# Kernel optimization log

Hardware: AMD Instinct MI355X
Metric: run time of the kernel (lower is better)

The kernel has to match this reference:

```python
import jax, jax.numpy as jnp
import numpy as np

DIM = 2048
HQ = 32
HKV = 8
HEAD_DIM = DIM // HQ          # 64
GROUP = HQ // HKV             # 4 q-heads per kv-head
B, S = 2, 2048


def setup_inputs() -> dict:
    key = jax.random.key(0)
    ks = jax.random.split(key, 12)
    sc_in = 1.0 / np.sqrt(DIM)   # lecun_normal fan-in scaling
    inp = {
        "q": jax.random.normal(ks[0], (B, S, DIM), jnp.float32),
        "k": jax.random.normal(ks[1], (B, S, DIM), jnp.float32),
        "v": jax.random.normal(ks[2], (B, S, DIM), jnp.float32),
        # causal 0/1 mask: module computes scores -= 1/mask + 1, so 0 -> -inf (masked), 1 -> -2 (softmax-invariant shift)
        "mask": jnp.tril(jnp.ones((S, S), jnp.int32)),
        "Wq": jax.random.normal(ks[3], (DIM, HQ * HEAD_DIM), jnp.float32) * sc_in,
        "bq": jnp.zeros((HQ * HEAD_DIM,), jnp.float32),
        "Wk": jax.random.normal(ks[4], (DIM, HKV * HEAD_DIM), jnp.float32) * sc_in,
        "bk": jnp.zeros((HKV * HEAD_DIM,), jnp.float32),
        "Wv": jax.random.normal(ks[5], (DIM, HKV * HEAD_DIM), jnp.float32) * sc_in,
        "bv": jnp.zeros((HKV * HEAD_DIM,), jnp.float32),
        "Wo": jax.random.normal(ks[6], (DIM, DIM), jnp.float32) * (1.0 / np.sqrt(DIM)),
        "bo": jnp.zeros((DIM,), jnp.float32),
    }
    return inp


def reference(q, k, v, mask, Wq, bq, Wk, bk, Wv, bv, Wo, bo):
    b, s, _ = q.shape
    # projections -> per-head layout
    qx = (q @ Wq + bq).reshape(b, s, HKV, GROUP, HEAD_DIM)   # grouped q-heads
    kx = (k @ Wk + bk).reshape(b, s, HKV, HEAD_DIM)
    vx = (v @ Wv + bv).reshape(b, s, HKV, HEAD_DIM)
    # scores[b, h, g, i, j] = q_i . k_j ; same math as repeating kv heads GROUP times
    scores = jnp.einsum('bihgd,bjhd->bhgij', qx, kx) / jnp.sqrt(
        jnp.asarray(HEAD_DIM, qx.dtype))
    # module's masking: scores -= 1/mask + 1  (mask==0 -> -inf, mask==1 -> -2)
    scores = scores - (1.0 / mask.astype(scores.dtype) + 1.0)
    probs = jax.nn.softmax(scores, axis=-1)
    out = jnp.einsum('bhgij,bjhd->bihgd', probs, vx).reshape(b, s, DIM)
    out = out @ Wo + bo
    return out
```

## Files before the change

kernel.cpp:

```cpp
#include <hip/hip_runtime.h>

typedef unsigned short u16;
typedef unsigned int u32;
typedef __attribute__((ext_vector_type(8))) short short8v;
typedef __attribute__((ext_vector_type(4))) float f32x4;

#define DIM 2048
#define HQN 32
#define HKVN 8
#define HD 64
#define BB 2
#define SS 2048
#define MTOT (BB*SS)
#define NKV (HKVN*HD)

__device__ __forceinline__ u16 f2bf(float f){
  u32 u = __float_as_uint(f);
  u += 0x7FFFu + ((u >> 16) & 1u);
  return (u16)(u >> 16);
}

__device__ __forceinline__ u32 cvtpk(float a, float b){
  u32 r; asm("v_cvt_pk_bf16_f32 %0, %1, %2" : "=v"(r) : "v"(a), "v"(b)); return r;
}

__device__ __forceinline__ void gload_lds16(const void* g, void* l){
  __builtin_amdgcn_global_load_lds((const __attribute__((address_space(1))) u32*)g,
                                   (__attribute__((address_space(3))) u32*)l, 16, 0, 0);
}

#define WAITVM_(N) asm volatile("s_waitcnt vmcnt(" #N ")" ::: "memory")
#define WAITVM(N) WAITVM_(N)
#define BARF()    do { asm volatile("" ::: "memory"); __builtin_amdgcn_s_barrier(); asm volatile("" ::: "memory"); } while(0)
#define MF(a,b,cc) __builtin_amdgcn_mfma_f32_16x16x32_bf16((a),(b),(cc),0,0,0)

__global__ __launch_bounds__(256) void cast3_kernel(const float4* __restrict__ q,
                                                    const float4* __restrict__ k,
                                                    const float4* __restrict__ v,
                                                    u16* __restrict__ qo,
                                                    u16* __restrict__ ko,
                                                    u16* __restrict__ vo, int n4){
  const int z = blockIdx.y;
  const float4* in = z==0 ? q : (z==1 ? k : v);
  u16* out = z==0 ? qo : (z==1 ? ko : vo);
  int i = blockIdx.x*256 + threadIdx.x;
  if (i < n4){
    float4 f = in[i];
    union { u16 s[4]; unsigned long long u; } r;
    r.s[0]=f2bf(f.x); r.s[1]=f2bf(f.y); r.s[2]=f2bf(f.z); r.s[3]=f2bf(f.w);
    *(unsigned long long*)(out + (size_t)i*4) = r.u;
  }
}

__global__ __launch_bounds__(256) void transpose4_kernel(const float* __restrict__ Wq,
                                                         const float* __restrict__ Wk,
                                                         const float* __restrict__ Wv,
                                                         const float* __restrict__ Wo,
                                                         u16* __restrict__ WqT,
                                                         u16* __restrict__ WkT,
                                                         u16* __restrict__ WvT,
                                                         u16* __restrict__ WoT){
  const int z = blockIdx.z;
  const float* W = z==0?Wq:(z==1?Wk:(z==2?Wv:Wo));
  u16* WT = z==0?WqT:(z==1?WkT:(z==2?WvT:WoT));
  const int N = (z==1||z==2) ? NKV : DIM;
  const int K = DIM;
  int n0 = blockIdx.x*32, k0 = blockIdx.y*32;
  if (n0 >= N) return;
  __shared__ float tile[32][33];
  int tx = threadIdx.x & 31, ty = threadIdx.x >> 5;
  #pragma unroll
  for (int i=0;i<4;i++){
    int kk = ty + i*8;
    tile[kk][tx] = W[(size_t)(k0+kk)*N + n0 + tx];
  }
  __syncthreads();
  #pragma unroll
  for (int i=0;i<4;i++){
    int n = ty + i*8;
    WT[(size_t)(n0+n)*K + k0 + tx] = f2bf(tile[tx][n]);
  }
}

__global__ __launch_bounds__(512, 1) void gemm_qkv_kernel(const u16* __restrict__ Aq,
                                                          const u16* __restrict__ Ak,
                                                          const u16* __restrict__ Av,
                                                          const u16* __restrict__ BT,
                                                          const float* __restrict__ bq,
                                                          const float* __restrict__ bk,
                                                          const float* __restrict__ bv,
                                                          u16* __restrict__ Qp,
                                                          u16* __restrict__ Kp,
                                                          u16* __restrict__ Vp){
  __shared__ __align__(16) u16 lds[65536];
  char* ldsb = (char*)lds;
  const int t = threadIdx.x, lane = t & 63, w = t >> 6;
  const int wm = w >> 2, wn = w & 3, g = lane >> 4, c = lane & 15;
  int bid = blockIdx.x;
  bid = (bid & 7)*24 + (bid >> 3);
  const int mt = bid / 12, nt = bid - mt*12;
  const int m0 = mt*256, n0 = nt*256;
  const int seg = (n0 >= 2560) ? 2 : (n0 >= 2048 ? 1 : 0);
  const u16* A = seg==0 ? Aq : (seg==1 ? Ak : Av);
  const float* bias = seg==0 ? bq : (seg==1 ? bk : bv);
  const int nbase = seg==0 ? 0 : (seg==1 ? 2048 : 2560);

  const int rA = t >> 3;
  const int kc = ((t & 7) ^ (rA & 7)) * 8;
  const u16* gA = A  + (size_t)(m0 + rA)*DIM + kc;
  const u16* gB = BT + (size_t)(n0 + ((rA>>5)<<6) + (rA & 31))*DIM + kc;

  const u32 ko0 = (u32)((g*16) ^ ((c&7)<<4));
  const u32 ko1 = (u32)((64 + g*16) ^ ((c&7)<<4));
  const u32 aoff = wm*8192 + c*128;
  const u32 boff = wn*4096 + c*128;

#define STGA_(PA, KT, ABASE) do{ \
    gload_lds16(gA + (size_t)(KT)*64 + (size_t)((PA)*64)*DIM,       ldsb + (ABASE) + (PA)*16384 + t*16); \
    gload_lds16(gA + (size_t)(KT)*64 + (size_t)((PA)*64+128)*DIM,   ldsb + (ABASE) + (PA)*16384 + 8192 + t*16); }while(0)
#define STGB_(PB, KT, BBASE) do{ \
    gload_lds16(gB + (size_t)(KT)*64 + (size_t)((PB)*32)*DIM,       ldsb + (BBASE) + (PB)*16384 + t*16); \
    gload_lds16(gB + (size_t)(KT)*64 + (size_t)((PB)*32+128)*DIM,   ldsb + (BBASE) + (PB)*16384 + 8192 + t*16); }while(0)
#define LD8(OFF) (*(const short8v*)(ldsb + (OFF)))

  const f32x4 fzero = {0.f,0.f,0.f,0.f};
  f32x4 acc[8][4];
  #pragma unroll
  for (int i=0;i<8;i++)
    #pragma unroll
    for (int j=0;j<4;j++) acc[i][j] = fzero;

#define RD_A(PABASE) do{ _Pragma("unroll") for (int q=0;q<4;q++){ \
    a_[q][0] = LD8((PABASE) + aoff + q*2048 + ko0); \
    a_[q][1] = LD8((PABASE) + aoff + q*2048 + ko1); } }while(0)
#define RD_B(DST, PBBASE) do{ _Pragma("unroll") for (int s=0;s<2;s++){ \
    DST[s][0] = LD8((PBBASE) + boff + s*2048 + ko0); \
    DST[s][1] = LD8((PBBASE) + boff + s*2048 + ko1); } }while(0)

#define MM16(BSRC, FM0, FN0) do{ __builtin_amdgcn_s_setprio(1); \
    _Pragma("unroll") for (int q=0;q<4;q++) \
      _Pragma("unroll") for (int s=0;s<2;s++){ \
        acc[(FM0)+q][(FN0)+s] = MF(a_[q][0], BSRC[s][0], acc[(FM0)+q][(FN0)+s]); \
        acc[(FM0)+q][(FN0)+s] = MF(a_[q][1], BSRC[s][1], acc[(FM0)+q][(FN0)+s]); } \
    __builtin_amdgcn_s_setprio(0); }while(0)

#define QSTEP(TT, CUR, DOSTG, TAIL) do{ \
    const u32 AC = (CUR)*32768,  BC2 = 65536 + (CUR)*32768; \
    const u32 AN = (CUR^1)*32768, BN2 = 65536 + (CUR^1)*32768; \
    short8v a_[4][2], b0_[2][2], b1_[2][2]; \
     \
    RD_A(AC); RD_B(b0_, BC2); \
    if (DOSTG) STGA_(0, (TT)+1, AN); \
    MM16(b0_, 0, 0); \
    if (TAIL) { WAITVM(2); } else { WAITVM(4); } \
    BARF(); \
     \
    RD_B(b1_, BC2 + 16384); \
    if (DOSTG) STGB_(0, (TT)+1, BN2); \
    MM16(b1_, 0, 2); \
    if (TAIL) { WAITVM(0); } else { WAITVM(4); } \
    BARF(); \
     \
    RD_A(AC + 16384); \
    if (DOSTG) STGB_(1, (TT)+1, BN2); \
    MM16(b1_, 4, 2); \
    BARF(); \
     \
    if (DOSTG) STGA_(1, (TT)+1, AN); \
    MM16(b0_, 4, 0); \
    if (!TAIL) { WAITVM(4); } \
    BARF(); \
  }while(0)

  STGA_(0, 0, 0); STGB_(0, 0, 65536); STGB_(1, 0, 65536); STGA_(1, 0, 0);
  WAITVM(4);
  BARF();

  #pragma unroll 1
  for (int tt = 0; tt < 30; tt += 2){
    QSTEP(tt,   0, 1, 0);
    QSTEP(tt+1, 1, 1, 0);
  }
  QSTEP(30, 0, 1, 0);
  QSTEP(31, 1, 0, 1);
#undef QSTEP

  WAITVM(0);
  __syncthreads();

  u16* st = lds + w*8192;
  if (seg == 2){
    #pragma unroll
    for (int fm=0; fm<8; fm++){
      #pragma unroll
      for (int fn=0; fn<4; fn++){
        float bvv = bias[n0 - nbase + wn*64 + fn*16 + c];
        int vbase = (fm>>1)*2048 + fn*512 + (g*16 + c)*8 + (fm&1)*4;
        *(u32*)&st[vbase]     = cvtpk(acc[fm][fn][0]+bvv, acc[fm][fn][1]+bvv);
        *(u32*)&st[vbase + 2] = cvtpk(acc[fm][fn][2]+bvv, acc[fm][fn][3]+bvv);
      }
    }
  } else {
    #pragma unroll
    for (int fm=0; fm<8; fm++){
      #pragma unroll
      for (int fn=0; fn<4; fn++){
        float bvv = bias[n0 - nbase + wn*64 + fn*16 + c];
        int sbase = (fm>>1)*2048 + ((fm&1)*2 + (fn>>1))*512 + (c>>2)*128 + (fn&1)*4 + (c&3);
        #pragma unroll
        for (int r=0; r<4; r++)
          st[sbase + (4*g + r)*8] = f2bf(acc[fm][fn][r] + bvv);
      }
    }
  }
  __syncthreads();
  {
    const int bb = m0 >> 11;
    const int st0 = ((m0 & 2047) >> 5) + wm*4;
    u16* dst;
    if (seg == 0)      dst = Qp + (((size_t)bb*HQN  + (n0>>6)        + wn) << 17);
    else if (seg == 1) dst = Kp + (((size_t)bb*HKVN + ((n0-2048)>>6) + wn) << 17);
    else               dst = Vp + (((size_t)bb*HKVN + ((n0-2560)>>6) + wn) << 17);
    dst += (size_t)st0*2048;
    #pragma unroll
    for (int i=0;i<16;i++)
      *(short8v*)(dst + lane*8 + i*512) = *(const short8v*)(st + lane*8 + i*512);
  }
#undef STGA_
#undef STGB_
#undef RD_A
#undef RD_B
#undef MM16
}

__global__ __launch_bounds__(512, 1) void gemm_o_kernel(const u16* __restrict__ A,
                                                        const u16* __restrict__ BT,
                                                        const float* __restrict__ bias,
                                                        float* __restrict__ C){
  __shared__ __align__(16) u16 lds[49152];
  char* ldsb = (char*)lds;
  const int t = threadIdx.x, lane = t & 63, w = t >> 6;
  const int wm = w >> 2, wn = w & 3, g = lane >> 4, c = lane & 15;
  int bid = blockIdx.x;
  bid = (bid & 7)*32 + (bid >> 3);
  const int m0 = (bid >> 4)*256, n0 = (bid & 15)*128;

  const int rA = t >> 3;
  const int kc = ((t & 7) ^ (rA & 7)) * 8;
  const u16* gA = A  + (size_t)(m0 + rA)*DIM + kc;
  const u16* gB = BT + (size_t)(n0 + rA)*DIM + kc;

  const u32 ko0 = (u32)((g*16) ^ ((c&7)<<4));
  const u32 ko1 = (u32)((64 + g*16) ^ ((c&7)<<4));
  const u32 aoff = wm*8192 + c*128;
  const u32 boffo = wn*4096 + c*128;

#define STGA_(PA, KT, ABASE) do{ \
    gload_lds16(gA + (size_t)(KT)*64 + (size_t)((PA)*64)*DIM,       ldsb + (ABASE) + (PA)*16384 + t*16); \
    gload_lds16(gA + (size_t)(KT)*64 + (size_t)((PA)*64+128)*DIM,   ldsb + (ABASE) + (PA)*16384 + 8192 + t*16); }while(0)
#define STGB_O(KT, BBASE) do{ \
    gload_lds16(gB + (size_t)(KT)*64,                     ldsb + (BBASE) + t*16); \
    gload_lds16(gB + (size_t)(KT)*64 + (size_t)64*DIM,    ldsb + (BBASE) + 8192 + t*16); }while(0)
#define LD8(OFF) (*(const short8v*)(ldsb + (OFF)))

  const f32x4 fzero = {0.f,0.f,0.f,0.f};
  f32x4 acc[8][2];
  #pragma unroll
  for (int i=0;i<8;i++){ acc[i][0] = fzero; acc[i][1] = fzero; }

#define RD_A(PABASE) do{ _Pragma("unroll") for (int q=0;q<4;q++){ \
    a_[q][0] = LD8((PABASE) + aoff + q*2048 + ko0); \
    a_[q][1] = LD8((PABASE) + aoff + q*2048 + ko1); } }while(0)
#define RD_BO(BBASE) do{ _Pragma("unroll") for (int s=0;s<2;s++){ \
    b_[s][0] = LD8((BBASE) + boffo + s*2048 + ko0); \
    b_[s][1] = LD8((BBASE) + boffo + s*2048 + ko1); } }while(0)

#define MMO(FM0) do{ __builtin_amdgcn_s_setprio(1); \
    _Pragma("unroll") for (int q=0;q<4;q++) \
      _Pragma("unroll") for (int s=0;s<2;s++){ \
        acc[(FM0)+q][s] = MF(a_[q][0], b_[s][0], acc[(FM0)+q][s]); \
        acc[(FM0)+q][s] = MF(a_[q][1], b_[s][1], acc[(FM0)+q][s]); } \
    __builtin_amdgcn_s_setprio(0); }while(0)

#define OSTEP(TT, CUR, DOSTG, TAIL) do{ \
    const u32 AC = (CUR)*32768,  BC2 = 65536 + (CUR)*16384; \
    const u32 AN = (CUR^1)*32768, BN2 = 65536 + (CUR^1)*16384; \
    short8v a_[4][2], b_[2][2]; \
     \
    RD_A(AC); RD_BO(BC2); \
    if (DOSTG) { STGA_(0, (TT)+1, AN); STGB_O((TT)+1, BN2); } \
    MMO(0); \
    if (TAIL) { WAITVM(0); } else { WAITVM(4); } \
    BARF(); \
     \
    RD_A(AC + 16384); \
    if (DOSTG) STGA_(1, (TT)+1, AN); \
    MMO(4); \
    if (!TAIL) { WAITVM(2); } \
    BARF(); \
  }while(0)

  STGA_(0, 0, 0); STGB_O(0, 65536); STGA_(1, 0, 0);
  WAITVM(2);
  BARF();

  #pragma unroll 1
  for (int tt = 0; tt < 30; tt += 2){
    OSTEP(tt,   0, 1, 0);
    OSTEP(tt+1, 1, 1, 0);
  }
  OSTEP(30, 0, 1, 0);
  OSTEP(31, 1, 0, 1);
#undef OSTEP

  #pragma unroll
  for (int fm=0; fm<8; fm++){
    #pragma unroll
    for (int s=0; s<2; s++){
      int n = n0 + wn*32 + s*16 + c;
      float bvv = bias[n];
      #pragma unroll
      for (int r=0; r<4; r++){
        int m = m0 + wm*128 + fm*16 + 4*g + r;
        C[(size_t)m*DIM + n] = acc[fm][s][r] + bvv;
      }
    }
  }
#undef STGA_
#undef STGB_O
#undef RD_A
#undef RD_BO
#undef MMO
}

__global__ __launch_bounds__(256) void attn_kernel(const u16* __restrict__ Qp,
                                                   const u16* __restrict__ Kp,
                                                   const u16* __restrict__ Vp,
                                                   u16* __restrict__ Aout){
  const int grp = blockIdx.x & 15;
  const int jj  = blockIdx.x >> 4;
  const int b   = grp >> 3;
  const int hkv = grp & 7;
  const int t = threadIdx.x;
  const int lane = t & 63, w = t >> 6;
  const int g = lane >> 4, c = lane & 15;
  const int hq = hkv*4 + w;

  __shared__ __align__(16) u16 ring[4][2][2048];

  const u16* Kb = Kp + (((size_t)b*HKVN + hkv) << 17);
  const u16* Vb = Vp + (((size_t)b*HKVN + hkv) << 17);
  const u16* Qb = Qp + (((size_t)b*HQN + hq) << 17);
  const float SCL = 0.18033688011112042f;
  const f32x4 fzero = {0.f,0.f,0.f,0.f};

  for (int half = 0; half < 2; ++half){
    const int T = half ? jj : (63 - jj);

    BARF();

    short8v qf[2][2];
    {
      const u16* qs = Qb + (size_t)T*2048 + lane*8;
      qf[0][0] = *(const short8v*)(qs);
      qf[0][1] = *(const short8v*)(qs + 512);
      qf[1][0] = *(const short8v*)(qs + 1024);
      qf[1][1] = *(const short8v*)(qs + 1536);
    }
    float l_r[2] = {0.f, 0.f};
    f32x4 o[2][4];
    #pragma unroll
    for (int qi=0; qi<2; qi++)
      #pragma unroll
      for (int f=0; f<4; f++) o[qi][f] = fzero;

    #pragma unroll
    for (int s=0; s<3; s++){
      const int tc = s > T ? T : s;
      gload_lds16(Kb + (size_t)tc*2048 + t*8, &ring[s][0][t*8]);
      gload_lds16(Vb + (size_t)tc*2048 + t*8, &ring[s][1][t*8]);
    }

    for (int kt = 0; kt <= T; ++kt){
      WAITVM(4);
      BARF();
      const int sl = kt & 3;
      short8v kf0 = *(const short8v*)&ring[sl][0][lane*8];
      short8v kf1 = *(const short8v*)&ring[sl][0][512 + lane*8];
      short8v kf2 = *(const short8v*)&ring[sl][0][1024 + lane*8];
      short8v kf3 = *(const short8v*)&ring[sl][0][1536 + lane*8];
      short8v vf0 = *(const short8v*)&ring[sl][1][lane*8];
      short8v vf1 = *(const short8v*)&ring[sl][1][512 + lane*8];
      short8v vf2 = *(const short8v*)&ring[sl][1][1024 + lane*8];
      short8v vf3 = *(const short8v*)&ring[sl][1][1536 + lane*8];
      {
        const int tc = (kt+3) > T ? T : (kt+3);
        const int sn = (kt+3) & 3;
        gload_lds16(Kb + (size_t)tc*2048 + t*8, &ring[sn][0][t*8]);
        gload_lds16(Vb + (size_t)tc*2048 + t*8, &ring[sn][1][t*8]);
      }
      const bool diag = (kt == T);
      #pragma unroll
      for (int qi=0; qi<2; qi++){
        f32x4 s0 = fzero, s1 = fzero;
        __builtin_amdgcn_s_setprio(1);
        s0 = MF(kf0, qf[qi][0], s0);
        s0 = MF(kf1, qf[qi][1], s0);
        s1 = MF(kf2, qf[qi][0], s1);
        s1 = MF(kf3, qf[qi][1], s1);
        __builtin_amdgcn_s_setprio(0);
        float p0[4], p1[4];
        #pragma unroll
        for (int r=0; r<4; r++){
          p0[r] = __builtin_amdgcn_exp2f(s0[r]*SCL);
          p1[r] = __builtin_amdgcn_exp2f(s1[r]*SCL);
        }
        if (diag){
          const int qloc = qi*16 + c;
          #pragma unroll
          for (int r=0; r<4; r++){
            if (4*g + r      > qloc) p0[r] = 0.f;
            if (16 + 4*g + r > qloc) p1[r] = 0.f;
          }
        }
        l_r[qi] += (p0[0]+p0[1]) + (p0[2]+p0[3]) + (p1[0]+p1[1]) + (p1[2]+p1[3]);
        union { u32 u[4]; short8v v; } pu;
        pu.u[0] = cvtpk(p0[0], p0[1]);
        pu.u[1] = cvtpk(p0[2], p0[3]);
        pu.u[2] = cvtpk(p1[0], p1[1]);
        pu.u[3] = cvtpk(p1[2], p1[3]);
        __builtin_amdgcn_s_setprio(1);
        o[qi][0] = MF(pu.v, vf0, o[qi][0]);
        o[qi][1] = MF(pu.v, vf1, o[qi][1]);
        o[qi][2] = MF(pu.v, vf2, o[qi][2]);
        o[qi][3] = MF(pu.v, vf3, o[qi][3]);
        __builtin_amdgcn_s_setprio(0);
      }
    }

    #pragma unroll
    for (int qi=0; qi<2; qi++){
      float ls = l_r[qi];
      ls += __shfl_xor(ls, 16);
      ls += __shfl_xor(ls, 32);
      float li = 1.0f / ls;
      float lf[4];
      #pragma unroll
      for (int r=0; r<4; r++) lf[r] = __shfl(li, 4*g + r);
      #pragma unroll
      for (int f=0; f<4; f++){
        #pragma unroll
        for (int r=0; r<4; r++){
          int q = T*32 + qi*16 + 4*g + r;
          Aout[((size_t)b*SS + q)*DIM + hq*HD + f*16 + c] = f2bf(o[qi][f][r]*lf[r]);
        }
      }
    }
  }
}

extern "C" void kernel_launch(void* const* d_in, const int* in_sizes, int n_in,
                              void* d_out, int out_size, void* d_ws, size_t ws_size,
                              hipStream_t stream){
  const float* q  = (const float*)d_in[0];
  const float* k  = (const float*)d_in[1];
  const float* v  = (const float*)d_in[2];
  const float* Wq = (const float*)d_in[4];
  const float* bq = (const float*)d_in[5];
  const float* Wk = (const float*)d_in[6];
  const float* bk = (const float*)d_in[7];
  const float* Wv = (const float*)d_in[8];
  const float* bv = (const float*)d_in[9];
  const float* Wo = (const float*)d_in[10];
  const float* bo = (const float*)d_in[11];
  float* out = (float*)d_out;

  char* ws = (char*)d_ws;
  u16* q_bf = (u16*)ws; ws += (size_t)MTOT*DIM*2;
  u16* k_bf = (u16*)ws; ws += (size_t)MTOT*DIM*2;
  u16* v_bf = (u16*)ws; ws += (size_t)MTOT*DIM*2;
  u16* WqT  = (u16*)ws; ws += (size_t)DIM*DIM*2;
  u16* WkT  = (u16*)ws; ws += (size_t)NKV*DIM*2;
  u16* WvT  = (u16*)ws; ws += (size_t)NKV*DIM*2;
  u16* WoT  = (u16*)ws; ws += (size_t)DIM*DIM*2;
  u16* Qp   = (u16*)ws; ws += (size_t)MTOT*DIM*2;
  u16* Kp   = (u16*)ws; ws += (size_t)MTOT*NKV*2;
  u16* Vp   = (u16*)ws; ws += (size_t)MTOT*NKV*2;
  u16* attn = (u16*)ws; ws += (size_t)MTOT*DIM*2;

  const int n4 = MTOT*DIM/4;
  cast3_kernel<<<dim3(n4/256, 3), 256, 0, stream>>>((const float4*)q, (const float4*)k,
                                                    (const float4*)v, q_bf, k_bf, v_bf, n4);
  transpose4_kernel<<<dim3(DIM/32, DIM/32, 4), 256, 0, stream>>>(Wq, Wk, Wv, Wo,
                                                                 WqT, WkT, WvT, WoT);
  gemm_qkv_kernel<<<192, 512, 0, stream>>>(q_bf, k_bf, v_bf, WqT,
                                           bq, bk, bv, Qp, Kp, Vp);
  attn_kernel<<<512, 256, 0, stream>>>(Qp, Kp, Vp, attn);
  gemm_o_kernel<<<256, 512, 0, stream>>>(attn, WoT, bo, out);
}
```

Before: 196.5 us.

## Split attention into one block per query tile and fold softmax scale into Q

The attention kernel used to process two balanced causal query tiles per block, (63-jj) and jj. It now launches 1024 blocks, each handling a single tile, ordered longest-first so the hardware scheduler can balance the work. The softmax scale (log2e/sqrt(d)) is applied to Q in the QKV GEMM epilogue, which removes a multiply per score. The K/V ring loop is unrolled by 4 so slot indices are compile-time constants. The cost is more blocks and reliance on launch order for load balance, and Q is rounded to bf16 after scaling.

```diff
diff --git a/kernel.cpp b/kernel.cpp
--- a/kernel.cpp
+++ b/kernel.cpp
@@ -13,6 +13,7 @@
 #define SS 2048
 #define MTOT (BB*SS)
 #define NKV (HKVN*HD)
+#define QSCL 0.18033688011112042f
 
 __device__ __forceinline__ u16 f2bf(float f){
   u32 u = __float_as_uint(f);
@@ -189,6 +190,7 @@
   __syncthreads();
 
   u16* st = lds + w*8192;
+  const float osc = (seg == 0) ? QSCL : 1.0f;
   if (seg == 2){
     #pragma unroll
     for (int fm=0; fm<8; fm++){
@@ -209,7 +211,7 @@
         int sbase = (fm>>1)*2048 + ((fm&1)*2 + (fn>>1))*512 + (c>>2)*128 + (fn&1)*4 + (c&3);
         #pragma unroll
         for (int r=0; r<4; r++)
-          st[sbase + (4*g + r)*8] = f2bf(acc[fm][fn][r] + bvv);
+          st[sbase + (4*g + r)*8] = f2bf((acc[fm][fn][r] + bvv)*osc);
       }
     }
   }
@@ -337,8 +339,9 @@
                                                    const u16* __restrict__ Kp,
                                                    const u16* __restrict__ Vp,
                                                    u16* __restrict__ Aout){
-  const int grp = blockIdx.x & 15;
-  const int jj  = blockIdx.x >> 4;
+  const int bid = blockIdx.x;
+  const int grp = bid & 15;
+  const int T   = 63 - (bid >> 4);
   const int b   = grp >> 3;
   const int hkv = grp & 7;
   const int t = threadIdx.x;
@@ -351,55 +354,52 @@
   const u16* Kb = Kp + (((size_t)b*HKVN + hkv) << 17);
   const u16* Vb = Vp + (((size_t)b*HKVN + hkv) << 17);
   const u16* Qb = Qp + (((size_t)b*HQN + hq) << 17);
-  const float SCL = 0.18033688011112042f;
   const f32x4 fzero = {0.f,0.f,0.f,0.f};
 
-  for (int half = 0; half < 2; ++half){
-    const int T = half ? jj : (63 - jj);
-
-    BARF();
-
-    short8v qf[2][2];
-    {
-      const u16* qs = Qb + (size_t)T*2048 + lane*8;
-      qf[0][0] = *(const short8v*)(qs);
-      qf[0][1] = *(const short8v*)(qs + 512);
-      qf[1][0] = *(const short8v*)(qs + 1024);
-      qf[1][1] = *(const short8v*)(qs + 1536);
-    }
-    float l_r[2] = {0.f, 0.f};
-    f32x4 o[2][4];
-    #pragma unroll
-    for (int qi=0; qi<2; qi++)
-      #pragma unroll
-      for (int f=0; f<4; f++) o[qi][f] = fzero;
-
-    #pragma unroll
-    for (int s=0; s<3; s++){
-      const int tc = s > T ? T : s;
-      gload_lds16(Kb + (size_t)tc*2048 + t*8, &ring[s][0][t*8]);
-      gload_lds16(Vb + (size_t)tc*2048 + t*8, &ring[s][1][t*8]);
-    }
-
-    for (int kt = 0; kt <= T; ++kt){
+  short8v qf[2][2];
+  {
+    const u16* qs = Qb + (size_t)T*2048 + lane*8;
+    qf[0][0] = *(const short8v*)(qs);
+    qf[0][1] = *(const short8v*)(qs + 512);
+    qf[1][0] = *(const short8v*)(qs + 1024);
+    qf[1][1] = *(const short8v*)(qs + 1536);
+  }
+  float l_r[2] = {0.f, 0.f};
+  f32x4 o[2][4];
+  #pragma unroll
+  for (int qi=0; qi<2; qi++)
+    #pragma unroll
+    for (int f=0; f<4; f++) o[qi][f] = fzero;
+
+  #pragma unroll
+  for (int s=0; s<3; s++){
+    const int tc = s > T ? T : s;
+    gload_lds16(Kb + (size_t)tc*2048 + t*8, &ring[s][0][t*8]);
+    gload_lds16(Vb + (size_t)tc*2048 + t*8, &ring[s][1][t*8]);
+  }
+
+  for (int kt = 0; kt <= T; kt += 4){
+    #pragma unroll
+    for (int s4 = 0; s4 < 4; ++s4){
+      const int kt_ = kt + s4;
+      if (kt_ > T) break;
       WAITVM(4);
       BARF();
-      const int sl = kt & 3;
-      short8v kf0 = *(const short8v*)&ring[sl][0][lane*8];
-      short8v kf1 = *(const short8v*)&ring[sl][0][512 + lane*8];
-      short8v kf2 = *(const short8v*)&ring[sl][0][1024 + lane*8];
-      short8v kf3 = *(const short8v*)&ring[sl][0][1536 + lane*8];
-      short8v vf0 = *(const short8v*)&ring[sl][1][lane*8];
-      short8v vf1 = *(const short8v*)&ring[sl][1][512 + lane*8];
-      short8v vf2 = *(const short8v*)&ring[sl][1][1024 + lane*8];
-      short8v vf3 = *(const short8v*)&ring[sl][1][1536 + lane*8];
+      short8v kf0 = *(const short8v*)&ring[s4][0][lane*8];
+      short8v kf1 = *(const short8v*)&ring[s4][0][512 + lane*8];
+      short8v kf2 = *(const short8v*)&ring[s4][0][1024 + lane*8];
+      short8v kf3 = *(const short8v*)&ring[s4][0][1536 + lane*8];
+      short8v vf0 = *(const short8v*)&ring[s4][1][lane*8];
+      short8v vf1 = *(const short8v*)&ring[s4][1][512 + lane*8];
+      short8v vf2 = *(const short8v*)&ring[s4][1][1024 + lane*8];
+      short8v vf3 = *(const short8v*)&ring[s4][1][1536 + lane*8];
       {
-        const int tc = (kt+3) > T ? T : (kt+3);
-        const int sn = (kt+3) & 3;
+        const int tc = (kt_+3) > T ? T : (kt_+3);
+        const int sn = (s4+3) & 3;
         gload_lds16(Kb + (size_t)tc*2048 + t*8, &ring[sn][0][t*8]);
         gload_lds16(Vb + (size_t)tc*2048 + t*8, &ring[sn][1][t*8]);
       }
-      const bool diag = (kt == T);
+      const bool diag = (kt_ == T);
       #pragma unroll
       for (int qi=0; qi<2; qi++){
         f32x4 s0 = fzero, s1 = fzero;
@@ -412,8 +412,8 @@
         float p0[4], p1[4];
         #pragma unroll
         for (int r=0; r<4; r++){
-          p0[r] = __builtin_amdgcn_exp2f(s0[r]*SCL);
-          p1[r] = __builtin_amdgcn_exp2f(s1[r]*SCL);
+          p0[r] = __builtin_amdgcn_exp2f(s0[r]);
+          p1[r] = __builtin_amdgcn_exp2f(s1[r]);
         }
         if (diag){
           const int qloc = qi*16 + c;
@@ -437,23 +437,23 @@
         __builtin_amdgcn_s_setprio(0);
       }
     }
-
-    #pragma unroll
-    for (int qi=0; qi<2; qi++){
-      float ls = l_r[qi];
-      ls += __shfl_xor(ls, 16);
-      ls += __shfl_xor(ls, 32);
-      float li = 1.0f / ls;
-      float lf[4];
+  }
+
+  #pragma unroll
+  for (int qi=0; qi<2; qi++){
+    float ls = l_r[qi];
+    ls += __shfl_xor(ls, 16);
+    ls += __shfl_xor(ls, 32);
+    float li = 1.0f / ls;
+    float lf[4];
+    #pragma unroll
+    for (int r=0; r<4; r++) lf[r] = __shfl(li, 4*g + r);
+    #pragma unroll
+    for (int f=0; f<4; f++){
       #pragma unroll
-      for (int r=0; r<4; r++) lf[r] = __shfl(li, 4*g + r);
-      #pragma unroll
-      for (int f=0; f<4; f++){
-        #pragma unroll
-        for (int r=0; r<4; r++){
-          int q = T*32 + qi*16 + 4*g + r;
-          Aout[((size_t)b*SS + q)*DIM + hq*HD + f*16 + c] = f2bf(o[qi][f][r]*lf[r]);
-        }
+      for (int r=0; r<4; r++){
+        int q = T*32 + qi*16 + 4*g + r;
+        Aout[((size_t)b*SS + q)*DIM + hq*HD + f*16 + c] = f2bf(o[qi][f][r]*lf[r]);
       }
     }
   }
@@ -495,6 +495,6 @@
                                                                  WqT, WkT, WvT, WoT);
   gemm_qkv_kernel<<<192, 512, 0, stream>>>(q_bf, k_bf, v_bf, WqT,
                                            bq, bk, bv, Qp, Kp, Vp);
-  attn_kernel<<<512, 256, 0, stream>>>(Qp, Kp, Vp, attn);
+  attn_kernel<<<1024, 256, 0, stream>>>(Qp, Kp, Vp, attn);
   gemm_o_kernel<<<256, 512, 0, stream>>>(attn, WoT, bo, out);
 }
```

Result: faster. 187.3 us (-4.7%).
